# Performance work log

Hardware: AMD Instinct MI355X
Metric: run time of the kernel (lower is better)

The kernel has to match this reference:

```python
import jax, jax.numpy as jnp
import numpy as np

B, C, N, T = 4, 16, 512, 64
P, Q = 10, 5  # s_order, t_order
C_OUT = 64
EPS = 1e-8
BN_EPS = 1e-5


def setup_inputs() -> dict:
    key = jax.random.key(0)
    ks = jax.random.split(key, 14)
    return {
        "x": jax.random.normal(ks[0], (B, C, N, T), jnp.float32),
        "sp_matrix": jax.random.normal(ks[1], (N, N), jnp.float32) / np.sqrt(N),
        "tp_matrix": jax.random.normal(ks[2], (T, T), jnp.float32) / np.sqrt(T),
        "STE": jax.random.normal(ks[3], (B, Q, P), jnp.float32),
        "w_t1": jax.random.normal(ks[4], (Q + 1, Q), jnp.float32) * 0.3,
        "b_t1": jax.random.normal(ks[5], (Q + 1,), jnp.float32) * 0.1,
        "w_t2": jax.random.normal(ks[6], (P + 1, P), jnp.float32) * 0.3,
        "b_t2": jax.random.normal(ks[7], (P + 1,), jnp.float32) * 0.1,
        "w_mlp": jax.random.normal(ks[8], (C_OUT, 2 * C), jnp.float32) * 0.1,
        "b_mlp": jax.random.normal(ks[9], (C_OUT,), jnp.float32) * 0.1,
        "bn_gamma": jnp.ones((C_OUT,), jnp.float32),
        "bn_beta": jnp.zeros((C_OUT,), jnp.float32),
        "bn_mean": jax.random.normal(ks[10], (C_OUT,), jnp.float32) * 0.1,
        "bn_var": jax.random.uniform(ks[11], (C_OUT,), jnp.float32) + 0.5,
    }


def _fro(a):
    # Frobenius norm over last two axes, keepdims, clamped
    return jnp.maximum(jnp.sqrt(jnp.sum(a * a, axis=(2, 3), keepdims=True)), EPS)


def _basis_s(L_s, last, second):
    rst = jnp.einsum('nm,bfmt->bfnt', L_s, last)
    rst = rst - jnp.sum(rst * last, axis=(2, 3), keepdims=True) * last
    rst = rst - jnp.sum(rst * second, axis=(2, 3), keepdims=True) * second
    return rst / _fro(rst)


def _basis_t(L_t, last, second):
    rst = jnp.einsum('bfnt,tu->bfnu', last, L_t)
    rst = rst - jnp.sum(rst * last, axis=(2, 3), keepdims=True) * last
    rst = rst - jnp.sum(rst * second, axis=(2, 3), keepdims=True) * second
    return rst / _fro(rst)


def _forward(x, sp_matrix, tp_matrix, STE, w_t1, b_t1, w_t2, b_t2,
             w_mlp, b_mlp, bn_gamma, bn_beta, bn_mean, bn_var):
    # theta: Conv1d(k=1) chains == matmuls over channel dims
    h = jnp.einsum('ot,bts->bos', w_t1, STE) + b_t1[None, :, None]   # [B,Q+1,P]
    h = jnp.transpose(h, (0, 2, 1))                                  # [B,P,Q+1]
    h = jnp.einsum('ps,bst->bpt', w_t2, h) + b_t2[None, :, None]     # [B,P+1,Q+1]
    h = jax.nn.relu(jnp.transpose(h, (0, 2, 1)))                     # [B,Q+1,P+1]
    theta = h.reshape(STE.shape[0], -1)                              # [B,(Q+1)(P+1)]

    m00 = x / _fro(x)
    zeros = jnp.zeros_like(x)
    last_s, sec_s = m00, zeros
    last_t, sec_t = m00, zeros
    M = [m00]
    for i in range(P + 1):
        if i > 0:
            mi0 = _basis_s(sp_matrix, last_s, sec_s)
            sec_s, last_s = last_s, mi0
            M.append(mi0)
            last_t, sec_t = mi0, zeros
        for _ in range(Q):
            mij = _basis_t(tp_matrix, last_t, sec_t)
            sec_t, last_t = last_t, mij
            M.append(mij)
    M = jnp.stack(M, axis=1)                                         # [B,R,C,N,T]

    x_st = jnp.einsum('br,brfnt->bfnt', theta, M)
    cat = jnp.concatenate([x, x_st], axis=1)                         # [B,2C,N,T]
    out = jnp.einsum('oc,bcnt->bont', w_mlp, cat) + b_mlp[None, :, None, None]
    # BatchNorm2d in eval mode (running stats); dropout is identity in eval
    inv = bn_gamma / jnp.sqrt(bn_var + BN_EPS)
    out = out * inv[None, :, None, None] + (bn_beta - bn_mean * inv)[None, :, None, None]
    return out


def reference(x, sp_matrix, tp_matrix, STE, w_t1, b_t1, w_t2, b_t2,
              w_mlp, b_mlp, bn_gamma, bn_beta, bn_mean, bn_var):
    return _forward(x, sp_matrix, tp_matrix, STE, w_t1, b_t1, w_t2, b_t2,
                    w_mlp, b_mlp, bn_gamma, bn_beta, bn_mean, bn_var)
```

## Files before the change

### kernel.cpp

```cpp
#include <hip/hip_runtime.h>
#include <hip/hip_bf16.h>

#define EPS 1e-8f

typedef short short8 __attribute__((ext_vector_type(8)));
typedef float f32x4 __attribute__((ext_vector_type(4)));
typedef unsigned short u16x4 __attribute__((ext_vector_type(4)));

#define OF_FLAG   0L
#define OF_THETA  16L
#define OF_SPH    4608L
#define OF_SPL    135680L
#define OF_BAR    266752L
#define OF_MI0    2363904L
#define OF_SCAL   25432576L
#define OF_XST    25434624L

__device__ inline float ld_in(const void* p, long i, int bf) {
  if (bf) return __bfloat162float(((const __hip_bfloat16*)p)[i]);
  return ((const float*)p)[i];
}

__device__ inline unsigned packw(float v) {
  unsigned u = __float_as_uint(v);
  unsigned h = u >> 16;
  float res = v - __uint_as_float(h << 16);
  return h | (__float_as_uint(res) & 0xFFFF0000u);
}

__device__ inline unsigned short bf16b(float v) {
  __hip_bfloat16 h = __float2bfloat16(v);
  return *(unsigned short*)&h;
}
__device__ inline float ubf(unsigned short u) {
  __hip_bfloat16 h = *(__hip_bfloat16*)&u;
  return __bfloat162float(h);
}
__device__ inline unsigned pk2(float a, float b) {
  return (unsigned)bf16b(a) | ((unsigned)bf16b(b) << 16);
}
__device__ inline float2 upk2(unsigned w) {
  return float2{ubf((unsigned short)(w & 0xFFFFu)), ubf((unsigned short)(w >> 16))};
}

__device__ inline void blk_reduce2(float& a, float& b, float* red) {
  #pragma unroll
  for (int off = 32; off > 0; off >>= 1) {
    a += __shfl_down(a, off, 64);
    b += __shfl_down(b, off, 64);
  }
  int w = threadIdx.x >> 6, lane = threadIdx.x & 63, nw = blockDim.x >> 6;
  __syncthreads();
  if (lane == 0) { red[w] = a; red[16 + w] = b; }
  __syncthreads();
  if (w == 0) {
    float sa = (lane < nw) ? red[lane] : 0.f;
    float sb = (lane < nw) ? red[16 + lane] : 0.f;
    #pragma unroll
    for (int off = 8; off > 0; off >>= 1) {
      sa += __shfl_down(sa, off, 64);
      sb += __shfl_down(sb, off, 64);
    }
    if (lane == 0) { red[32] = sa; red[33] = sb; }
  }
  __syncthreads();
  a = red[32]; b = red[33];
}

__device__ inline void blk_reduce1(float& a, float* red) {
  #pragma unroll
  for (int off = 32; off > 0; off >>= 1) a += __shfl_down(a, off, 64);
  int w = threadIdx.x >> 6, lane = threadIdx.x & 63, nw = blockDim.x >> 6;
  __syncthreads();
  if (lane == 0) red[w] = a;
  __syncthreads();
  if (w == 0) {
    float sa = (lane < nw) ? red[lane] : 0.f;
    #pragma unroll
    for (int off = 8; off > 0; off >>= 1) sa += __shfl_down(sa, off, 64);
    if (lane == 0) red[32] = sa;
  }
  __syncthreads();
  a = red[32];
}

__global__ void k0_theta(const void* ste, const void* w1, const void* b1,
                         const void* w2, const void* b2, const void* gamma,
                         float* ws) {
  __shared__ int sflag;
  int tid = threadIdx.x;
  if (tid == 0) {
    unsigned bits = ((const unsigned*)gamma)[0];
    int f = (bits == 0x3F800000u) ? 0 : 1;
    sflag = f;
    ((int*)ws)[OF_FLAG] = f;
  }
  __syncthreads();
  int bf = sflag;
  if (tid < 264) {
    int b = tid / 66, r = tid % 66, o = r / 11, p = r % 11;
    float acc = ld_in(b2, p, bf);
    for (int s = 0; s < 10; ++s) {
      float h1 = ld_in(b1, o, bf);
      for (int t = 0; t < 5; ++t)
        h1 += ld_in(w1, o * 5 + t, bf) * ld_in(ste, (long)(b * 5 + t) * 10 + s, bf);
      acc += ld_in(w2, p * 10 + s, bf) * h1;
    }
    ws[OF_THETA + b * 66 + r] = fmaxf(acc, 0.f);
  }
  for (int q = tid; q < 2048; q += blockDim.x) ws[OF_SCAL + q] = 0.f;
  int* bi = (int*)(ws + OF_BAR);
  for (int q = tid; q < 704; q += blockDim.x) bi[q] = 0;
}

__global__ void k_conv(const void* sp, float* ws) {
  int bf = ((const int*)ws)[0];
  int i = blockIdx.x * 1024 + threadIdx.x;
  int e = i & 7, c = (i >> 3) & 15, qd = (i >> 7) & 3, kc = (i >> 9) & 15, ng2 = i >> 13;
  long src = (long)(ng2 * 16 + c) * 512 + kc * 32 + qd * 8 + e;
  unsigned wv = packw(ld_in(sp, src, bf));
  ((unsigned short*)(ws + OF_SPH))[i] = (unsigned short)(wv & 0xFFFFu);
  ((unsigned short*)(ws + OF_SPL))[i] = (unsigned short)(wv >> 16);
}

__global__ __launch_bounds__(1024) void k_nrm0(const void* x, float* ws) {
  __shared__ float red[34];
  int slice = blockIdx.x, tid = threadIdx.x;
  int bf = ((const int*)ws)[0];
  long soff = (long)slice * 32768;
  float s = 0.f;
  #pragma unroll
  for (int k = 0; k < 32; ++k) { float v = ld_in(x, soff + k * 1024 + tid, bf); s += v * v; }
  blk_reduce1(s, red);
  if (tid == 0) ws[OF_SCAL + slice] = s;
}

__global__ __launch_bounds__(256) void k_scaleT(const void* x, float* ws) {
  __shared__ float tile[64 * 65];
  int bid = blockIdx.x, tid = threadIdx.x;
  int slice = bid >> 3, nb = bid & 7;
  int bf = ((const int*)ws)[0];
  long soff = (long)slice * 32768;
  for (int q = 0; q < 16; ++q) {
    int idx = q * 256 + tid;
    int nl = idx >> 6, t = idx & 63;
    tile[nl * 65 + t] = ld_in(x, soff + (long)(nb * 64 + nl) * 64 + t, bf);
  }
  __syncthreads();
  float* mi = ws + OF_MI0 + soff;
  for (int q = 0; q < 16; ++q) {
    int idx = q * 256 + tid;
    int t = idx >> 6, nl = idx & 63;
    mi[t * 512 + nb * 64 + nl] = tile[nl * 65 + t];
  }
}

__global__ __launch_bounds__(1024, 4) void ck1(float* ws) {
  __shared__ float RBv[2][16 * 516];
  __shared__ __align__(16) unsigned short Wh[16 * 520];
  __shared__ __align__(16) unsigned short Wl[16 * 520];
  __shared__ float red[44];
  int tid = threadIdx.x, bid = blockIdx.x;
  int slice = (bid & 7) * 8 + (bid >> 5);
  int tb = (bid >> 3) & 3;
  long soff = (long)slice * 32768;
  int w = tid >> 6, lane = tid & 63, quad = lane >> 4, col = lane & 15;
  int n0 = w * 32 + col, n1 = n0 + 16;
  int tlA = tid >> 7, m4 = tid & 127;
  const unsigned short* sph = (const unsigned short*)(ws + OF_SPH);
  const unsigned short* spl = (const unsigned short*)(ws + OF_SPL);
  int* bar = (int*)(ws + OF_BAR);

  float4 pv[2], pv2[2];
  pv[0] = float4{0.f, 0.f, 0.f, 0.f};  pv[1] = pv[0];
  pv2[0] = pv[0];                      pv2[1] = pv[0];

  for (int i = 1; i <= 11; ++i) {
    int cur = i & 1;
    float alpha = 0.f, beta = 0.f;
    if (i >= 2) {
      if (tid == 0) {
        int* slot = bar + (i - 2) * 64 + slice;
        __hip_atomic_fetch_add(slot, 1, __ATOMIC_RELEASE, __HIP_MEMORY_SCOPE_AGENT);
        while (__hip_atomic_load(slot, __ATOMIC_ACQUIRE, __HIP_MEMORY_SCOPE_AGENT) < 4)
          __builtin_amdgcn_s_sleep(1);
        float nq = __hip_atomic_load(&ws[OF_SCAL + (i - 2) * 64 + slice],
                                     __ATOMIC_RELAXED, __HIP_MEMORY_SCOPE_AGENT);
        float dA = __hip_atomic_load(&ws[OF_SCAL + 704 + (i - 2) * 64 + slice],
                                     __ATOMIC_RELAXED, __HIP_MEMORY_SCOPE_AGENT);
        red[40] = dA / fmaxf(nq, 1e-30f);
        float bb = 0.f;
        if (i >= 3) {
          float nq3 = __hip_atomic_load(&ws[OF_SCAL + (i - 3) * 64 + slice],
                                        __ATOMIC_RELAXED, __HIP_MEMORY_SCOPE_AGENT);
          float dB = __hip_atomic_load(&ws[OF_SCAL + 1344 + (i - 3) * 64 + slice],
                                       __ATOMIC_RELAXED, __HIP_MEMORY_SCOPE_AGENT);
          bb = dB / fmaxf(nq3, 1e-30f);
        }
        red[41] = bb;
      }
      __syncthreads();
      alpha = red[40]; beta = red[41];
    }

    float npp = 0.f;
    #pragma unroll
    for (int q = 0; q < 2; ++q) {
      int tl = tlA + q * 8;
      int lo = tl * 516 + m4 * 4;
      float4 v;
      if (i == 1) {
        v = *(const float4*)(ws + OF_MI0 + soff + (long)(tb * 16 + tl) * 512 + m4 * 4);
      } else {
        float4 r = *(const float4*)&RBv[cur][lo];
        v.x = r.x - alpha * pv[q].x - beta * pv2[q].x;
        v.y = r.y - alpha * pv[q].y - beta * pv2[q].y;
        v.z = r.z - alpha * pv[q].z - beta * pv2[q].z;
        v.w = r.w - alpha * pv[q].w - beta * pv2[q].w;
        *(float4*)(ws + OF_MI0 + (long)(i - 1) * 2097152 + soff
                   + (long)(tb * 16 + tl) * 512 + m4 * 4) = v;
        npp += v.x * v.x + v.y * v.y + v.z * v.z + v.w * v.w;
      }
      *(float4*)&RBv[cur][lo] = v;
      pv2[q] = pv[q]; pv[q] = v;
      if (i <= 10) {
        unsigned p0 = packw(v.x), p1 = packw(v.y), p2 = packw(v.z), p3 = packw(v.w);
        u16x4 hv = { (unsigned short)(p0 & 0xFFFFu), (unsigned short)(p1 & 0xFFFFu),
                     (unsigned short)(p2 & 0xFFFFu), (unsigned short)(p3 & 0xFFFFu) };
        u16x4 lv = { (unsigned short)(p0 >> 16), (unsigned short)(p1 >> 16),
                     (unsigned short)(p2 >> 16), (unsigned short)(p3 >> 16) };
        *(u16x4*)&Wh[tl * 520 + m4 * 4] = hv;
        *(u16x4*)&Wl[tl * 520 + m4 * 4] = lv;
      }
    }
    if (i >= 2) {
      blk_reduce1(npp, red);
      if (tid == 0) atomicAdd(ws + OF_SCAL + (i - 1) * 64 + slice, npp);
    } else {
      __syncthreads();
    }
    if (i == 11) break;

    f32x4 C0 = {0.f, 0.f, 0.f, 0.f}, C1 = {0.f, 0.f, 0.f, 0.f};
    #pragma unroll 4
    for (int kc = 0; kc < 16; ++kc) {
      short8 ah = *(const short8*)&Wh[col * 520 + kc * 32 + quad * 8];
      short8 al = *(const short8*)&Wl[col * 520 + kc * 32 + quad * 8];
      long ob0 = (((long)(w * 2) * 16 + kc) * 64 + quad * 16 + col) * 8;
      long ob1 = (((long)(w * 2 + 1) * 16 + kc) * 64 + quad * 16 + col) * 8;
      short8 bh0 = *(const short8*)(sph + ob0);
      short8 bl0 = *(const short8*)(spl + ob0);
      short8 bh1 = *(const short8*)(sph + ob1);
      short8 bl1 = *(const short8*)(spl + ob1);
      C0 = __builtin_amdgcn_mfma_f32_16x16x32_bf16(ah, bh0, C0, 0, 0, 0);
      C0 = __builtin_amdgcn_mfma_f32_16x16x32_bf16(ah, bl0, C0, 0, 0, 0);
      C0 = __builtin_amdgcn_mfma_f32_16x16x32_bf16(al, bh0, C0, 0, 0, 0);
      C1 = __builtin_amdgcn_mfma_f32_16x16x32_bf16(ah, bh1, C1, 0, 0, 0);
      C1 = __builtin_amdgcn_mfma_f32_16x16x32_bf16(ah, bl1, C1, 0, 0, 0);
      C1 = __builtin_amdgcn_mfma_f32_16x16x32_bf16(al, bh1, C1, 0, 0, 0);
    }

    float d1p = 0.f, d2p = 0.f;
    #pragma unroll
    for (int r = 0; r < 4; ++r) {
      int tl = quad * 4 + r;
      float lv0 = RBv[cur][tl * 516 + n0];
      float lv1 = RBv[cur][tl * 516 + n1];
      d1p += C0[r] * lv0 + C1[r] * lv1;
      if (i >= 2)
        d2p += C0[r] * RBv[cur ^ 1][tl * 516 + n0] + C1[r] * RBv[cur ^ 1][tl * 516 + n1];
      RBv[cur ^ 1][tl * 516 + n0] = C0[r];
      RBv[cur ^ 1][tl * 516 + n1] = C1[r];
    }
    blk_reduce2(d1p, d2p, red);
    if (tid == 0) {
      atomicAdd(ws + OF_SCAL + 704 + (i - 1) * 64 + slice, d1p);
      if (i >= 2) atomicAdd(ws + OF_SCAL + 1344 + (i - 2) * 64 + slice, d2p);
    }
  }
}

__global__ __launch_bounds__(1024, 4) void k2m(float* ws, const void* tp) {
  __shared__ unsigned LW[2][16384];
  __shared__ unsigned AH[2048];
  __shared__ float red[24];
  int tid = threadIdx.x;
  int slice = blockIdx.x / 11, ic = blockIdx.x % 11;
  int b = slice >> 4;
  int w = tid >> 6, lane = tid & 63, quad = lane >> 4, col = lane & 15;
  int mt = w & 3, ng = w >> 2;
  int bf = ((const int*)ws)[0];

  #pragma unroll
  for (int s = 0; s < 2; ++s) {
    int widx = s * 1024 + tid;
    int tq_ = widx & 3, ln = (widx >> 2) & 63, ktm = widx >> 8;
    int kt_ = ktm & 1, mt_ = ktm >> 1;
    int qd = ln >> 4, cl = ln & 15;
    int ua = mt_ * 16 + cl;
    int t0 = kt_ * 32 + qd * 8 + tq_ * 2;
    AH[widx] = pk2(ld_in(tp, (long)t0 * 64 + ua, bf),
                   ld_in(tp, (long)(t0 + 1) * 64 + ua, bf));
  }
  if (tid < 24) red[tid] = 0.f;

  float rinv = 1.f / fmaxf(sqrtf(ws[OF_SCAL + ic * 64 + slice]), EPS);
  float* seed = ws + OF_MI0 + (long)ic * 2097152 + (long)slice * 32768;

  for (int q = 0; q < 16; ++q) {
    int widx = q * 1024 + tid;
    int tpair = widx >> 9, n = widx & 511;
    float v0 = seed[(2 * tpair) * 512 + n] * rinv;
    float v1 = seed[(2 * tpair + 1) * 512 + n] * rinv;
    int li = ((tpair >> 2) * 512 + n) * 4 + (tpair & 3);
    LW[0][li] = pk2(v0, v1);
    LW[1][widx] = 0u;
  }
  __syncthreads();

  int t8c = mt * 2 + (quad >> 1);
  int tq0 = (quad * 2) & 3;
  float c0 = ws[OF_THETA + b * 66 + ic * 6 + 0];

  unsigned accP[16];
  #pragma unroll
  for (int nti = 0; nti < 8; ++nti) {
    int nn = ng * 128 + nti * 16 + col;
    int base = (t8c * 512 + nn) * 4;
    uint2 lw = *(uint2*)&LW[0][base + tq0];
    float2 p01 = upk2(lw.x), p23 = upk2(lw.y);
    accP[nti * 2] = pk2(c0 * p01.x, c0 * p01.y);
    accP[nti * 2 + 1] = pk2(c0 * p23.x, c0 * p23.y);
  }

  unsigned* cur = &LW[0][0];
  unsigned* prv = &LW[1][0];

  for (int j = 1; j <= 5; ++j) {
    f32x4 C[8];
    #pragma unroll
    for (int nti = 0; nti < 8; ++nti) C[nti] = (f32x4){0.f, 0.f, 0.f, 0.f};
    #pragma unroll
    for (int kt = 0; kt < 2; ++kt) {
      short8 a = *(short8*)&AH[((mt * 2 + kt) * 64 + lane) * 4];
      #pragma unroll
      for (int nti = 0; nti < 8; ++nti) {
        int bn = ng * 128 + nti * 16 + col;
        short8 bb = *(short8*)&cur[((kt * 4 + quad) * 512 + bn) * 4];
        C[nti] = __builtin_amdgcn_mfma_f32_16x16x32_bf16(a, bb, C[nti], 0, 0, 0);
      }
    }
    uint2 rlc[8], rlp[8];
    float d1p = 0.f, d2p = 0.f, nrm = 0.f;
    #pragma unroll
    for (int nti = 0; nti < 8; ++nti) {
      int nn = ng * 128 + nti * 16 + col;
      int base = (t8c * 512 + nn) * 4;
      rlc[nti] = *(uint2*)&cur[base + tq0];
      rlp[nti] = *(uint2*)&prv[base + tq0];
      float2 l01 = upk2(rlc[nti].x), l23 = upk2(rlc[nti].y);
      float2 s01 = upk2(rlp[nti].x), s23 = upk2(rlp[nti].y);
      d1p += C[nti][0] * l01.x + C[nti][1] * l01.y + C[nti][2] * l23.x + C[nti][3] * l23.y;
      d2p += C[nti][0] * s01.x + C[nti][1] * s01.y + C[nti][2] * s23.x + C[nti][3] * s23.y;
      nrm += C[nti][0] * C[nti][0] + C[nti][1] * C[nti][1]
           + C[nti][2] * C[nti][2] + C[nti][3] * C[nti][3];
    }
    #pragma unroll
    for (int off = 32; off > 0; off >>= 1) {
      d1p += __shfl_down(d1p, off, 64);
      d2p += __shfl_down(d2p, off, 64);
      nrm += __shfl_down(nrm, off, 64);
    }
    if (lane == 0) {
      atomicAdd(&red[j * 4 + 0], d1p);
      atomicAdd(&red[j * 4 + 1], d2p);
      atomicAdd(&red[j * 4 + 2], nrm);
    }
    __syncthreads();
    float d1 = red[j * 4 + 0], d2 = red[j * 4 + 1], nr = red[j * 4 + 2];
    float np = fmaxf(nr - d1 * d1 - d2 * d2, 0.f);
    float ri = 1.f / fmaxf(sqrtf(np), EPS);
    float cj = ws[OF_THETA + b * 66 + ic * 6 + j];
    #pragma unroll
    for (int nti = 0; nti < 8; ++nti) {
      int nn = ng * 128 + nti * 16 + col;
      int base = (t8c * 512 + nn) * 4;
      float2 l01 = upk2(rlc[nti].x), l23 = upk2(rlc[nti].y);
      float2 s01 = upk2(rlp[nti].x), s23 = upk2(rlp[nti].y);
      float vh0 = (C[nti][0] - d1 * l01.x - d2 * s01.x) * ri;
      float vh1 = (C[nti][1] - d1 * l01.y - d2 * s01.y) * ri;
      float vh2 = (C[nti][2] - d1 * l23.x - d2 * s23.x) * ri;
      float vh3 = (C[nti][3] - d1 * l23.y - d2 * s23.y) * ri;
      float2 a0 = upk2(accP[nti * 2]), a1 = upk2(accP[nti * 2 + 1]);
      accP[nti * 2] = pk2(a0.x + cj * vh0, a0.y + cj * vh1);
      accP[nti * 2 + 1] = pk2(a1.x + cj * vh2, a1.y + cj * vh3);
      uint2 nw; nw.x = pk2(vh0, vh1); nw.y = pk2(vh2, vh3);
      *(uint2*)&prv[base + tq0] = nw;
    }
    unsigned* t = cur; cur = prv; prv = t;
    __syncthreads();
  }
  float* po = seed;
  #pragma unroll
  for (int nti = 0; nti < 8; ++nti) {
    int nn = ng * 128 + nti * 16 + col;
    int u0 = mt * 16 + quad * 4;
    float2 a0 = upk2(accP[nti * 2]), a1 = upk2(accP[nti * 2 + 1]);
    po[(u0 + 0) * 512 + nn] = a0.x;
    po[(u0 + 1) * 512 + nn] = a0.y;
    po[(u0 + 2) * 512 + nn] = a1.x;
    po[(u0 + 3) * 512 + nn] = a1.y;
  }
}

__global__ __launch_bounds__(256) void k2r(float* ws) {
  long i = ((long)blockIdx.x * 256 + threadIdx.x) * 4;
  float4 s = *(const float4*)(ws + OF_MI0 + i);
  #pragma unroll
  for (int ic = 1; ic <= 10; ++ic) {
    float4 v = *(const float4*)(ws + OF_MI0 + (long)ic * 2097152 + i);
    s.x += v.x; s.y += v.y; s.z += v.z; s.w += v.w;
  }
  *(float4*)(ws + OF_XST + i) = s;
}

__global__ __launch_bounds__(1024) void k3(const void* x, const void* wmlp, const void* bmlp,
    const void* gam, const void* bet, const void* mea, const void* var,
    const float* ws, void* out) {
  __shared__ float wA[64 * 16], wB[64 * 16], winv[64], wsh[64], wb[64];
  __shared__ float tile[16 * 64 * 17];
  int tid = threadIdx.x, bid = blockIdx.x;
  int bf = ((const int*)ws)[0];
  int b = bid >> 5, nbase = (bid & 31) * 16;
  if (tid < 64) {
    float g = ld_in(gam, tid, bf), vv = ld_in(var, tid, bf);
    float iv = g / sqrtf(vv + 1e-5f);
    winv[tid] = iv;
    wsh[tid] = ld_in(bet, tid, bf) - ld_in(mea, tid, bf) * iv;
    wb[tid] = ld_in(bmlp, tid, bf);
  }
  for (int q = tid; q < 2048; q += 1024) {
    int o = q >> 5, c = q & 31;
    float v = ld_in(wmlp, q, bf);
    if (c < 16) wA[o * 16 + c] = v; else wB[o * 16 + (c - 16)] = v;
  }
  const float* xst = ws + OF_XST;
  #pragma unroll
  for (int q = 0; q < 4; ++q) {
    int idx = q * 1024 + tid;
    int f = idx >> 8, t = (idx >> 2) & 63, dn4 = idx & 3;
    float4 v = *(const float4*)(xst + ((long)(b * 16 + f)) * 32768 + t * 512 + nbase + dn4 * 4);
    float* dst = tile + f * 1088 + t * 17 + dn4 * 4;
    dst[0] = v.x; dst[1] = v.y; dst[2] = v.z; dst[3] = v.w;
  }
  __syncthreads();
  long pos = (long)(bid & 31) * 1024 + tid;
  int t = tid & 63, nl = tid >> 6;
  float xv[16], av[16];
  #pragma unroll
  for (int c = 0; c < 16; ++c)
    xv[c] = ld_in(x, ((long)(b * 16 + c)) * 32768 + pos, bf);
  #pragma unroll
  for (int f = 0; f < 16; ++f)
    av[f] = tile[f * 1088 + t * 17 + nl];
  #pragma unroll 4
  for (int o = 0; o < 64; ++o) {
    float s = wb[o];
    #pragma unroll
    for (int c = 0; c < 16; ++c) s += wA[o * 16 + c] * xv[c];
    #pragma unroll
    for (int f = 0; f < 16; ++f) s += wB[o * 16 + f] * av[f];
    s = s * winv[o] + wsh[o];
    long oi = ((long)(b * 64 + o)) * 32768 + pos;
    if (bf) ((__hip_bfloat16*)out)[oi] = __float2bfloat16(s);
    else ((float*)out)[oi] = s;
  }
}

extern "C" void kernel_launch(void* const* d_in, const int* in_sizes, int n_in,
                              void* d_out, int out_size, void* d_ws, size_t ws_size,
                              hipStream_t stream) {
  (void)in_sizes; (void)n_in; (void)out_size; (void)ws_size;
  float* ws = (float*)d_ws;

  k0_theta<<<1, 320, 0, stream>>>(d_in[3], d_in[4], d_in[5], d_in[6], d_in[7], d_in[10], ws);
  k_conv<<<256, 1024, 0, stream>>>(d_in[1], ws);
  k_nrm0<<<64, 1024, 0, stream>>>(d_in[0], ws);
  k_scaleT<<<512, 256, 0, stream>>>(d_in[0], ws);
  ck1<<<256, 1024, 0, stream>>>(ws);
  k2m<<<704, 1024, 0, stream>>>(ws, d_in[2]);
  k2r<<<2048, 256, 0, stream>>>(ws);
  k3<<<128, 1024, 0, stream>>>(d_in[0], d_in[8], d_in[9], d_in[10], d_in[11], d_in[12], d_in[13],
                               ws, d_out);
}
```

Measured before the change: 444.0 us.

## Derive basis norms algebraically, halve k2m LDS, fuse reduction into k3

ck1 stops reducing the squared norm of each new basis vector across the block. It instead computes that norm algebraically from ||L v||^2 minus the projection terms, and ||L v||^2 is reduced together with the dot products using wave shuffles plus shared atomics. This removes one block-wide reduction and several barriers per iteration. k2m drops its double-buffered LDS by keeping the previous vector in registers, which lets the launch bound allow 8 waves per CU. The separate k2r summation kernel is folded into k3's tile load, removing a launch and one round trip of the summed tensor through memory. The algebraic norm can lose precision through cancellation, which the code partly guards with a clamp at zero.

```diff
diff --git a/kernel.cpp b/kernel.cpp
--- a/kernel.cpp
+++ b/kernel.cpp
@@ -12,9 +12,9 @@
 #define OF_SPH    4608L
 #define OF_SPL    135680L
 #define OF_BAR    266752L
+#define OF_NRR    267776L
 #define OF_MI0    2363904L
 #define OF_SCAL   25432576L
-#define OF_XST    25434624L
 
 __device__ inline float ld_in(const void* p, long i, int bf) {
   if (bf) return __bfloat162float(((const __hip_bfloat16*)p)[i]);
@@ -41,30 +41,6 @@
 }
 __device__ inline float2 upk2(unsigned w) {
   return float2{ubf((unsigned short)(w & 0xFFFFu)), ubf((unsigned short)(w >> 16))};
-}
-
-__device__ inline void blk_reduce2(float& a, float& b, float* red) {
-  #pragma unroll
-  for (int off = 32; off > 0; off >>= 1) {
-    a += __shfl_down(a, off, 64);
-    b += __shfl_down(b, off, 64);
-  }
-  int w = threadIdx.x >> 6, lane = threadIdx.x & 63, nw = blockDim.x >> 6;
-  __syncthreads();
-  if (lane == 0) { red[w] = a; red[16 + w] = b; }
-  __syncthreads();
-  if (w == 0) {
-    float sa = (lane < nw) ? red[lane] : 0.f;
-    float sb = (lane < nw) ? red[16 + lane] : 0.f;
-    #pragma unroll
-    for (int off = 8; off > 0; off >>= 1) {
-      sa += __shfl_down(sa, off, 64);
-      sb += __shfl_down(sb, off, 64);
-    }
-    if (lane == 0) { red[32] = sa; red[33] = sb; }
-  }
-  __syncthreads();
-  a = red[32]; b = red[33];
 }
 
 __device__ inline void blk_reduce1(float& a, float* red) {
@@ -111,6 +87,7 @@
   for (int q = tid; q < 2048; q += blockDim.x) ws[OF_SCAL + q] = 0.f;
   int* bi = (int*)(ws + OF_BAR);
   for (int q = tid; q < 704; q += blockDim.x) bi[q] = 0;
+  for (int q = tid; q < 640; q += blockDim.x) ws[OF_NRR + q] = 0.f;
 }
 
 __global__ void k_conv(const void* sp, float* ws) {
@@ -159,7 +136,7 @@
   __shared__ float RBv[2][16 * 516];
   __shared__ __align__(16) unsigned short Wh[16 * 520];
   __shared__ __align__(16) unsigned short Wl[16 * 520];
-  __shared__ float red[44];
+  __shared__ float red[8];
   int tid = threadIdx.x, bid = blockIdx.x;
   int slice = (bid & 7) * 8 + (bid >> 5);
   int tb = (bid >> 3) & 3;
@@ -174,6 +151,7 @@
   float4 pv[2], pv2[2];
   pv[0] = float4{0.f, 0.f, 0.f, 0.f};  pv[1] = pv[0];
   pv2[0] = pv[0];                      pv2[1] = pv[0];
+  float h1 = 0.f, h2 = 0.f;
 
   for (int i = 1; i <= 11; ++i) {
     int cur = i & 1;
@@ -184,26 +162,31 @@
         __hip_atomic_fetch_add(slot, 1, __ATOMIC_RELEASE, __HIP_MEMORY_SCOPE_AGENT);
         while (__hip_atomic_load(slot, __ATOMIC_ACQUIRE, __HIP_MEMORY_SCOPE_AGENT) < 4)
           __builtin_amdgcn_s_sleep(1);
-        float nq = __hip_atomic_load(&ws[OF_SCAL + (i - 2) * 64 + slice],
-                                     __ATOMIC_RELAXED, __HIP_MEMORY_SCOPE_AGENT);
         float dA = __hip_atomic_load(&ws[OF_SCAL + 704 + (i - 2) * 64 + slice],
                                      __ATOMIC_RELAXED, __HIP_MEMORY_SCOPE_AGENT);
-        red[40] = dA / fmaxf(nq, 1e-30f);
+        float nr = __hip_atomic_load(&ws[OF_NRR + (i - 2) * 64 + slice],
+                                     __ATOMIC_RELAXED, __HIP_MEMORY_SCOPE_AGENT);
+        float a = dA / fmaxf(h1, 1e-30f);
         float bb = 0.f;
+        float nsqNew = nr - a * dA;
         if (i >= 3) {
-          float nq3 = __hip_atomic_load(&ws[OF_SCAL + (i - 3) * 64 + slice],
-                                        __ATOMIC_RELAXED, __HIP_MEMORY_SCOPE_AGENT);
           float dB = __hip_atomic_load(&ws[OF_SCAL + 1344 + (i - 3) * 64 + slice],
                                        __ATOMIC_RELAXED, __HIP_MEMORY_SCOPE_AGENT);
-          bb = dB / fmaxf(nq3, 1e-30f);
+          bb = dB / fmaxf(h2, 1e-30f);
+          nsqNew -= bb * dB;
         }
-        red[41] = bb;
+        nsqNew = fmaxf(nsqNew, 0.f);
+        red[4] = a; red[5] = bb;
+        if (tb == 0) ws[OF_SCAL + (i - 1) * 64 + slice] = nsqNew;
+        h2 = h1; h1 = nsqNew;
       }
       __syncthreads();
-      alpha = red[40]; beta = red[41];
-    }
-
-    float npp = 0.f;
+      alpha = red[4]; beta = red[5];
+    } else {
+      if (tid == 0) h1 = ws[OF_SCAL + slice];
+    }
+    if (tid < 4) red[tid] = 0.f;
+
     #pragma unroll
     for (int q = 0; q < 2; ++q) {
       int tl = tlA + q * 8;
@@ -219,7 +202,6 @@
         v.w = r.w - alpha * pv[q].w - beta * pv2[q].w;
         *(float4*)(ws + OF_MI0 + (long)(i - 1) * 2097152 + soff
                    + (long)(tb * 16 + tl) * 512 + m4 * 4) = v;
-        npp += v.x * v.x + v.y * v.y + v.z * v.z + v.w * v.w;
       }
       *(float4*)&RBv[cur][lo] = v;
       pv2[q] = pv[q]; pv[q] = v;
@@ -233,13 +215,8 @@
         *(u16x4*)&Wl[tl * 520 + m4 * 4] = lv;
       }
     }
-    if (i >= 2) {
-      blk_reduce1(npp, red);
-      if (tid == 0) atomicAdd(ws + OF_SCAL + (i - 1) * 64 + slice, npp);
-    } else {
-      __syncthreads();
-    }
     if (i == 11) break;
+    __syncthreads();
 
     f32x4 C0 = {0.f, 0.f, 0.f, 0.f}, C1 = {0.f, 0.f, 0.f, 0.f};
     #pragma unroll 4
@@ -260,7 +237,7 @@
       C1 = __builtin_amdgcn_mfma_f32_16x16x32_bf16(al, bh1, C1, 0, 0, 0);
     }
 
-    float d1p = 0.f, d2p = 0.f;
+    float d1p = 0.f, d2p = 0.f, nrr = 0.f;
     #pragma unroll
     for (int r = 0; r < 4; ++r) {
       int tl = quad * 4 + r;
@@ -269,19 +246,32 @@
       d1p += C0[r] * lv0 + C1[r] * lv1;
       if (i >= 2)
         d2p += C0[r] * RBv[cur ^ 1][tl * 516 + n0] + C1[r] * RBv[cur ^ 1][tl * 516 + n1];
+      nrr += C0[r] * C0[r] + C1[r] * C1[r];
       RBv[cur ^ 1][tl * 516 + n0] = C0[r];
       RBv[cur ^ 1][tl * 516 + n1] = C1[r];
     }
-    blk_reduce2(d1p, d2p, red);
+    #pragma unroll
+    for (int off = 32; off > 0; off >>= 1) {
+      d1p += __shfl_down(d1p, off, 64);
+      d2p += __shfl_down(d2p, off, 64);
+      nrr += __shfl_down(nrr, off, 64);
+    }
+    if (lane == 0) {
+      atomicAdd(&red[0], d1p);
+      atomicAdd(&red[1], d2p);
+      atomicAdd(&red[2], nrr);
+    }
+    __syncthreads();
     if (tid == 0) {
-      atomicAdd(ws + OF_SCAL + 704 + (i - 1) * 64 + slice, d1p);
-      if (i >= 2) atomicAdd(ws + OF_SCAL + 1344 + (i - 2) * 64 + slice, d2p);
-    }
-  }
-}
-
-__global__ __launch_bounds__(1024, 4) void k2m(float* ws, const void* tp) {
-  __shared__ unsigned LW[2][16384];
+      atomicAdd(ws + OF_SCAL + 704 + (i - 1) * 64 + slice, red[0]);
+      if (i >= 2) atomicAdd(ws + OF_SCAL + 1344 + (i - 2) * 64 + slice, red[1]);
+      atomicAdd(ws + OF_NRR + (i - 1) * 64 + slice, red[2]);
+    }
+  }
+}
+
+__global__ __launch_bounds__(1024, 8) void k2m(float* ws, const void* tp) {
+  __shared__ unsigned LW[16384];
   __shared__ unsigned AH[2048];
   __shared__ float red[24];
   int tid = threadIdx.x;
@@ -313,8 +303,7 @@
     float v0 = seed[(2 * tpair) * 512 + n] * rinv;
     float v1 = seed[(2 * tpair + 1) * 512 + n] * rinv;
     int li = ((tpair >> 2) * 512 + n) * 4 + (tpair & 3);
-    LW[0][li] = pk2(v0, v1);
-    LW[1][widx] = 0u;
+    LW[li] = pk2(v0, v1);
   }
   __syncthreads();
 
@@ -323,18 +312,17 @@
   float c0 = ws[OF_THETA + b * 66 + ic * 6 + 0];
 
   unsigned accP[16];
+  uint2 nwprev[8];
   #pragma unroll
   for (int nti = 0; nti < 8; ++nti) {
     int nn = ng * 128 + nti * 16 + col;
     int base = (t8c * 512 + nn) * 4;
-    uint2 lw = *(uint2*)&LW[0][base + tq0];
+    uint2 lw = *(uint2*)&LW[base + tq0];
     float2 p01 = upk2(lw.x), p23 = upk2(lw.y);
     accP[nti * 2] = pk2(c0 * p01.x, c0 * p01.y);
     accP[nti * 2 + 1] = pk2(c0 * p23.x, c0 * p23.y);
-  }
-
-  unsigned* cur = &LW[0][0];
-  unsigned* prv = &LW[1][0];
+    nwprev[nti] = uint2{0u, 0u};
+  }
 
   for (int j = 1; j <= 5; ++j) {
     f32x4 C[8];
@@ -346,20 +334,19 @@
       #pragma unroll
       for (int nti = 0; nti < 8; ++nti) {
         int bn = ng * 128 + nti * 16 + col;
-        short8 bb = *(short8*)&cur[((kt * 4 + quad) * 512 + bn) * 4];
+        short8 bb = *(short8*)&LW[((kt * 4 + quad) * 512 + bn) * 4];
         C[nti] = __builtin_amdgcn_mfma_f32_16x16x32_bf16(a, bb, C[nti], 0, 0, 0);
       }
     }
-    uint2 rlc[8], rlp[8];
     float d1p = 0.f, d2p = 0.f, nrm = 0.f;
     #pragma unroll
     for (int nti = 0; nti < 8; ++nti) {
       int nn = ng * 128 + nti * 16 + col;
       int base = (t8c * 512 + nn) * 4;
-      rlc[nti] = *(uint2*)&cur[base + tq0];
-      rlp[nti] = *(uint2*)&prv[base + tq0];
-      float2 l01 = upk2(rlc[nti].x), l23 = upk2(rlc[nti].y);
-      float2 s01 = upk2(rlp[nti].x), s23 = upk2(rlp[nti].y);
+      uint2 lc = *(uint2*)&LW[base + tq0];
+      uint2 lp = nwprev[nti];
+      float2 l01 = upk2(lc.x), l23 = upk2(lc.y);
+      float2 s01 = upk2(lp.x), s23 = upk2(lp.y);
       d1p += C[nti][0] * l01.x + C[nti][1] * l01.y + C[nti][2] * l23.x + C[nti][3] * l23.y;
       d2p += C[nti][0] * s01.x + C[nti][1] * s01.y + C[nti][2] * s23.x + C[nti][3] * s23.y;
       nrm += C[nti][0] * C[nti][0] + C[nti][1] * C[nti][1]
@@ -385,8 +372,10 @@
     for (int nti = 0; nti < 8; ++nti) {
       int nn = ng * 128 + nti * 16 + col;
       int base = (t8c * 512 + nn) * 4;
-      float2 l01 = upk2(rlc[nti].x), l23 = upk2(rlc[nti].y);
-      float2 s01 = upk2(rlp[nti].x), s23 = upk2(rlp[nti].y);
+      uint2 lc = *(uint2*)&LW[base + tq0];
+      uint2 lp = nwprev[nti];
+      float2 l01 = upk2(lc.x), l23 = upk2(lc.y);
+      float2 s01 = upk2(lp.x), s23 = upk2(lp.y);
       float vh0 = (C[nti][0] - d1 * l01.x - d2 * s01.x) * ri;
       float vh1 = (C[nti][1] - d1 * l01.y - d2 * s01.y) * ri;
       float vh2 = (C[nti][2] - d1 * l23.x - d2 * s23.x) * ri;
@@ -395,9 +384,9 @@
       accP[nti * 2] = pk2(a0.x + cj * vh0, a0.y + cj * vh1);
       accP[nti * 2 + 1] = pk2(a1.x + cj * vh2, a1.y + cj * vh3);
       uint2 nw; nw.x = pk2(vh0, vh1); nw.y = pk2(vh2, vh3);
-      *(uint2*)&prv[base + tq0] = nw;
-    }
-    unsigned* t = cur; cur = prv; prv = t;
+      *(uint2*)&LW[base + tq0] = nw;
+      nwprev[nti] = lc;
+    }
     __syncthreads();
   }
   float* po = seed;
@@ -411,17 +400,6 @@
     po[(u0 + 2) * 512 + nn] = a1.x;
     po[(u0 + 3) * 512 + nn] = a1.y;
   }
-}
-
-__global__ __launch_bounds__(256) void k2r(float* ws) {
-  long i = ((long)blockIdx.x * 256 + threadIdx.x) * 4;
-  float4 s = *(const float4*)(ws + OF_MI0 + i);
-  #pragma unroll
-  for (int ic = 1; ic <= 10; ++ic) {
-    float4 v = *(const float4*)(ws + OF_MI0 + (long)ic * 2097152 + i);
-    s.x += v.x; s.y += v.y; s.z += v.z; s.w += v.w;
-  }
-  *(float4*)(ws + OF_XST + i) = s;
 }
 
 __global__ __launch_bounds__(1024) void k3(const void* x, const void* wmlp, const void* bmlp,
@@ -444,14 +422,19 @@
     float v = ld_in(wmlp, q, bf);
     if (c < 16) wA[o * 16 + c] = v; else wB[o * 16 + (c - 16)] = v;
   }
-  const float* xst = ws + OF_XST;
   #pragma unroll
   for (int q = 0; q < 4; ++q) {
     int idx = q * 1024 + tid;
     int f = idx >> 8, t = (idx >> 2) & 63, dn4 = idx & 3;
-    float4 v = *(const float4*)(xst + ((long)(b * 16 + f)) * 32768 + t * 512 + nbase + dn4 * 4);
+    long off = ((long)(b * 16 + f)) * 32768 + t * 512 + nbase + dn4 * 4;
+    float4 s = float4{0.f, 0.f, 0.f, 0.f};
+    #pragma unroll
+    for (int ic = 0; ic <= 10; ++ic) {
+      float4 v = *(const float4*)(ws + OF_MI0 + (long)ic * 2097152 + off);
+      s.x += v.x; s.y += v.y; s.z += v.z; s.w += v.w;
+    }
     float* dst = tile + f * 1088 + t * 17 + dn4 * 4;
-    dst[0] = v.x; dst[1] = v.y; dst[2] = v.z; dst[3] = v.w;
+    dst[0] = s.x; dst[1] = s.y; dst[2] = s.z; dst[3] = s.w;
   }
   __syncthreads();
   long pos = (long)(bid & 31) * 1024 + tid;
@@ -489,7 +472,6 @@
   k_scaleT<<<512, 256, 0, stream>>>(d_in[0], ws);
   ck1<<<256, 1024, 0, stream>>>(ws);
   k2m<<<704, 1024, 0, stream>>>(ws, d_in[2]);
-  k2r<<<2048, 256, 0, stream>>>(ws);
   k3<<<128, 1024, 0, stream>>>(d_in[0], d_in[8], d_in[9], d_in[10], d_in[11], d_in[12], d_in[13],
                                ws, d_out);
 }
```

Result: slower. 674.0 us (+51.8%).
